# Performance work log

Measured on AMD Instinct MI355X. Metric: run time of the kernel, lower is better.

## Reference

```python
import jax, jax.numpy as jnp
import numpy as np

N, H, W = 128, 192, 192
THING = 81            # cfg.MODEL.SOGNET.THING_NUM_CLASSES
CLS_DIM = 128         # cls_embedding_dim
POS_DIM = 64          # pos_embedding_dim
REL_DIM = CLS_DIM + POS_DIM


def setup_inputs() -> dict:
    key = jax.random.key(0)
    ks = jax.random.split(key, 8)
    mask_logits = jax.random.normal(ks[0], (1, N, H, W), dtype=jnp.float32)
    # valid boxes: x_max > x_min, y_max > y_min (log(w/h) must be finite)
    xy = jax.random.uniform(ks[1], (N, 2), minval=0.0, maxval=800.0)
    wh = jax.random.uniform(ks[2], (N, 2), minval=16.0, maxval=256.0)
    bbox = jnp.concatenate([xy, xy + wh], axis=1).astype(jnp.float32)
    cls_idx = jax.random.randint(ks[3], (N,), 1, THING)  # values in [1, 80]
    # params (kaiming-normal-ish scale)
    W_U = jax.random.normal(ks[4], (THING - 1, CLS_DIM), jnp.float32) * (2.0 / (THING - 1)) ** 0.5
    W_V = jax.random.normal(ks[5], (THING - 1, CLS_DIM), jnp.float32) * (2.0 / (THING - 1)) ** 0.5
    W_pos = jax.random.normal(ks[6], (4, POS_DIM), jnp.float32) * (2.0 / 4.0) ** 0.5
    W_P = jax.random.normal(ks[7], (REL_DIM, 1), jnp.float32) * (2.0 / REL_DIM) ** 0.5
    return {"mask_logits": mask_logits, "bbox": bbox, "W_U": W_U, "W_V": W_V,
            "W_pos": W_pos, "W_P": W_P, "cls_idx": cls_idx}


def _position_matrix(bbox):
    x_min, y_min, x_max, y_max = bbox[:, 0], bbox[:, 1], bbox[:, 2], bbox[:, 3]
    w = x_max - x_min
    h = y_max - y_min
    x_ctr = (x_min + x_max) / 2.0
    y_ctr = (y_min + y_max) / 2.0
    dx = -(x_ctr[:, None] - x_ctr[None, :]) / w[:, None]          # [N, N]
    dy = -(y_ctr[:, None] - y_ctr[None, :]) / h[:, None]
    dw = jnp.log(w[None, :] / w[:, None])                          # log(w_j / w_i)
    dh = jnp.log(h[None, :] / h[:, None])
    return jnp.stack([dx, dy, dw, dh], axis=2)                     # [N, N, 4]


def reference(mask_logits, bbox, W_U, W_V, W_pos, W_P, cls_idx):
    # --- class relation: outer product of two relu'd class embeddings ---
    one_hot = jax.nn.one_hot(cls_idx - 1, THING - 1, dtype=mask_logits.dtype)  # [N, 80]
    feat1 = jax.nn.relu(one_hot @ W_U)                             # [N, CLS_DIM]
    feat2 = jax.nn.relu(one_hot @ W_V)
    cls_rel = feat1[:, None, :] * feat2[None, :, :]                # [N, N, CLS_DIM]
    # --- position relation: 1x1 conv == linear over last dim ---
    pos_rel = jax.nn.relu(jnp.einsum('ijk,kd->ijd', _position_matrix(bbox), W_pos))  # [N, N, POS_DIM]
    # --- relation score ---
    relation_feat = jnp.concatenate([cls_rel, pos_rel], axis=2)    # [N, N, REL_DIM]
    overlap_score = jax.nn.sigmoid(jnp.einsum('ijk,k->ij', relation_feat, W_P[:, 0]))  # [N, N]
    relation_score = jax.nn.relu(overlap_score - overlap_score.T)  # [N, N]
    # --- relation-weighted mask aggregation ---
    # naive: sum_m (ml*mp)[b,n] * mp[b,m] * score[n,m]  -> factor the m-reduction as a GEMM
    mask_prob = jax.nn.sigmoid(mask_logits)                        # [1, N, H, W]
    weighted = jnp.einsum('nm,bmhw->bnhw', relation_score, mask_prob)
    overlap_part = mask_logits * mask_prob * weighted              # [1, N, H, W]
    return mask_logits - overlap_part
```

## Files before the change

### kernel.cpp

```cpp
#include <hip/hip_runtime.h>

#define HW    36864
#define PX    144
#define RST   136

typedef unsigned short u16;
typedef unsigned int   u32;
typedef __attribute__((ext_vector_type(8))) short bf16x8;
typedef __attribute__((ext_vector_type(4))) float f32x4;

__device__ __forceinline__ float bf2f(u32 u) {
    union { u32 i; float f; } c; c.i = u << 16; return c.f;
}
__device__ __forceinline__ u16 f2bf(float f) {
    union { float f; u32 i; } c; c.f = f;
    u32 r = (c.i + 0x7fffu + ((c.i >> 16) & 1u)) >> 16;
    return (u16)r;
}
__device__ __forceinline__ u32 pack2(float a, float b) {
    return (u32)f2bf(a) | ((u32)f2bf(b) << 16);
}
__device__ __forceinline__ float sigf(float x) { return 1.0f / (1.0f + __expf(-x)); }

__device__ __forceinline__ void unpack8(uint4 v, float* o) {
    o[0] = bf2f(v.x & 0xffffu); o[1] = bf2f(v.x >> 16);
    o[2] = bf2f(v.y & 0xffffu); o[3] = bf2f(v.y >> 16);
    o[4] = bf2f(v.z & 0xffffu); o[5] = bf2f(v.z >> 16);
    o[6] = bf2f(v.w & 0xffffu); o[7] = bf2f(v.w >> 16);
}

template<int BF16>
__device__ __forceinline__ float ld1(const void* p, int idx) {
    return BF16 ? bf2f((u32)((const u16*)p)[idx]) : ((const float*)p)[idx];
}

template<int BF16>
__device__ __forceinline__ bool wrong_dtype(const void* ml, int tid) {
    int pred = 0;
    if (tid < 128) {
        u16 v = ((const u16*)ml)[tid];
        u32 e = (v >> 7) & 0xffu;
        pred = ((v & 0x7fffu) == 0 || (e >= 90u && e <= 140u)) ? 1 : 0;
    }
    int cnt = __syncthreads_count(pred);
    return (cnt >= 100) != (BF16 != 0);
}

template<int BF16>
__global__ __launch_bounds__(128) void k_rel(
    const void* __restrict__ ml,   const void* __restrict__ bbox,
    const void* __restrict__ WU,   const void* __restrict__ WV,
    const void* __restrict__ Wpos, const void* __restrict__ WP,
    const int* __restrict__ cls,   u16* __restrict__ relN)
{
    const int n = blockIdx.x, m = threadIdx.x;
    if (wrong_dtype<BF16>(ml, m)) return;

    __shared__ float u_s[128], v_s[128], wpos_s[256], wpp_s[64], bbn_s[4];

    const int cn = cls[n] - 1;
    {
        float wp = ld1<BF16>(WP, m);
        u_s[m] = fmaxf(ld1<BF16>(WU, cn * 128 + m), 0.f) * wp;
        v_s[m] = fmaxf(ld1<BF16>(WV, cn * 128 + m), 0.f) * wp;
    }
    wpos_s[m]       = ld1<BF16>(Wpos, m);
    wpos_s[128 + m] = ld1<BF16>(Wpos, 128 + m);
    if (m < 64) wpp_s[m] = ld1<BF16>(WP, 128 + m);
    if (m < 4)  bbn_s[m] = ld1<BF16>(bbox, n * 4 + m);
    __syncthreads();

    const int cm = cls[m] - 1;
    float s1 = 0.f, s2 = 0.f;
    #pragma unroll 8
    for (int c = 0; c < 128; ++c) {
        float wv = ld1<BF16>(WV, cm * 128 + c);
        float wu = ld1<BF16>(WU, cm * 128 + c);
        s1 += u_s[c] * fmaxf(wv, 0.f);
        s2 += v_s[c] * fmaxf(wu, 0.f);
    }

    const float xmn = bbn_s[0], ymn = bbn_s[1], xMn = bbn_s[2], yMn = bbn_s[3];
    const float wn = xMn - xmn, hn = yMn - ymn;
    const float xcn = 0.5f * (xmn + xMn), ycn = 0.5f * (ymn + yMn);
    const float xmm = ld1<BF16>(bbox, m * 4 + 0), ymm = ld1<BF16>(bbox, m * 4 + 1);
    const float xMm = ld1<BF16>(bbox, m * 4 + 2), yMm = ld1<BF16>(bbox, m * 4 + 3);
    const float wm = xMm - xmm, hm = yMm - ymm;
    const float xcm = 0.5f * (xmm + xMm), ycm = 0.5f * (ymm + yMm);

    const float p0 = -(xcn - xcm) / wn, p1 = -(ycn - ycm) / hn;
    const float p2 = __logf(wm / wn),   p3 = __logf(hm / hn);
    const float q0 = -(xcm - xcn) / wm, q1 = -(ycm - ycn) / hm;
    const float q2 = __logf(wn / wm),   q3 = __logf(hn / hm);

    #pragma unroll 8
    for (int d = 0; d < 64; ++d) {
        float w0 = wpos_s[d], w1 = wpos_s[64 + d], w2 = wpos_s[128 + d], w3 = wpos_s[192 + d];
        float wp = wpp_s[d];
        float t1 = p0 * w0 + p1 * w1 + p2 * w2 + p3 * w3;
        float t2 = q0 * w0 + q1 * w1 + q2 * w2 + q3 * w3;
        s1 += fmaxf(t1, 0.f) * wp;
        s2 += fmaxf(t2, 0.f) * wp;
    }

    float r = fmaxf(sigf(s1) - sigf(s2), 0.f);
    relN[n * 128 + m] = f2bf(r);
}

template<int BF16>
__global__ __launch_bounds__(256) void k_main(
    const void* __restrict__ mlv, const u16* __restrict__ relN,
    void* __restrict__ outv)
{
    const int tid = threadIdx.x;
    if (wrong_dtype<BF16>(mlv, tid)) return;

    __shared__ u16 rel_s[128 * RST];
    __shared__ u16 prob_s[64 * PX];

    const int px0 = blockIdx.x * PX;
    const int w    = tid >> 6;
    const int lane = tid & 63;
    const int col  = lane & 15;
    const int quad = lane >> 4;
    const int n0   = w * 32;

    for (int idx = tid; idx < 2048; idx += 256) {
        int r = idx >> 4, c = idx & 15;
        uint4 v = ((const uint4*)relN)[idx];
        *(uint4*)(rel_s + r * RST + c * 8) = v;
    }

    f32x4 acc[2][9];
    #pragma unroll
    for (int i = 0; i < 2; ++i)
        #pragma unroll
        for (int t = 0; t < 9; ++t) acc[i][t] = (f32x4){0.f, 0.f, 0.f, 0.f};

    for (int h = 0; h < 2; ++h) {
        __syncthreads();
        for (int idx = tid; idx < 1152; idx += 256) {
            int r = idx / 18, c = idx - r * 18;
            size_t base = (size_t)(h * 64 + r) * HW + px0 + c * 8;
            float f[8];
            if (BF16) {
                uint4 v = *(const uint4*)((const u16*)mlv + base);
                unpack8(v, f);
            } else {
                float4 v0 = *(const float4*)((const float*)mlv + base);
                float4 v1 = *(const float4*)((const float*)mlv + base + 4);
                f[0] = v0.x; f[1] = v0.y; f[2] = v0.z; f[3] = v0.w;
                f[4] = v1.x; f[5] = v1.y; f[6] = v1.z; f[7] = v1.w;
            }
            uint4 o;
            o.x = pack2(sigf(f[0]), sigf(f[1]));
            o.y = pack2(sigf(f[2]), sigf(f[3]));
            o.z = pack2(sigf(f[4]), sigf(f[5]));
            o.w = pack2(sigf(f[6]), sigf(f[7]));
            *(uint4*)(prob_s + r * PX + c * 8) = o;
        }
        __syncthreads();

        #pragma unroll
        for (int ksl = 0; ksl < 2; ++ksl) {
            const int k0 = h * 64 + ksl * 32 + quad * 8;
            bf16x8 a0 = *(const bf16x8*)(rel_s + (n0 + col) * RST + k0);
            bf16x8 a1 = *(const bf16x8*)(rel_s + (n0 + 16 + col) * RST + k0);
            const u16* bbase = prob_s + (ksl * 32 + quad * 8) * PX + col;
            #pragma unroll
            for (int t = 0; t < 9; ++t) {
                const u16* bp = bbase + t * 16;
                bf16x8 bfrag;
                #pragma unroll
                for (int j = 0; j < 8; ++j) bfrag[j] = (short)bp[j * PX];
                acc[0][t] = __builtin_amdgcn_mfma_f32_16x16x32_bf16(a0, bfrag, acc[0][t], 0, 0, 0);
                acc[1][t] = __builtin_amdgcn_mfma_f32_16x16x32_bf16(a1, bfrag, acc[1][t], 0, 0, 0);
            }
        }
    }

    #pragma unroll
    for (int i = 0; i < 2; ++i) {
        #pragma unroll
        for (int t = 0; t < 9; ++t) {
            const int nb = n0 + i * 16 + quad * 4;
            const int px = px0 + t * 16 + col;
            #pragma unroll
            for (int r = 0; r < 4; ++r) {
                size_t off = (size_t)(nb + r) * HW + px;
                float mlvv = BF16 ? bf2f((u32)((const u16*)mlv)[off])
                                  : ((const float*)mlv)[off];
                float pr = sigf(mlvv);
                float o  = mlvv - mlvv * pr * acc[i][t][r];
                if (BF16) ((u16*)outv)[off] = f2bf(o);
                else      ((float*)outv)[off] = o;
            }
        }
    }
}

extern "C" void kernel_launch(void* const* d_in, const int* in_sizes, int n_in,
                              void* d_out, int out_size, void* d_ws, size_t ws_size,
                              hipStream_t stream) {
    const void* ml   = d_in[0];
    const void* bbox = d_in[1];
    const void* WU   = d_in[2];
    const void* WV   = d_in[3];
    const void* Wpos = d_in[4];
    const void* WP   = d_in[5];
    const int*  cls  = (const int*)d_in[6];

    u16* relN = (u16*)d_ws;

    k_rel<1><<<dim3(128), dim3(128), 0, stream>>>(ml, bbox, WU, WV, Wpos, WP, cls, relN);
    k_rel<0><<<dim3(128), dim3(128), 0, stream>>>(ml, bbox, WU, WV, Wpos, WP, cls, relN);
    k_main<1><<<dim3(256), dim3(256), 0, stream>>>(ml, relN, d_out);
    k_main<0><<<dim3(256), dim3(256), 0, stream>>>(ml, relN, d_out);
}
```

Before: 105.7 us.

## Merge dtype variants, precompute class dot table, shrink pixel tiles with swizzled LDS

Replaces the two templated dtype kernels with single kernels that branch at runtime, cutting four launches to two. The class-relation dot products are computed once per row as an 80-entry table built with wave reductions, instead of a 128-long serial loop per thread. The main kernel's pixel tile drops from 144 to 64 columns, so the grid grows from 256 to 576 blocks. Its LDS probability tile uses an XOR swizzle to reduce bank conflicts, and launch bounds request two blocks per CU. The cost is that each block reloads the full relation matrix, and there are more blocks in total.

```diff
diff --git a/kernel.cpp b/kernel.cpp
--- a/kernel.cpp
+++ b/kernel.cpp
@@ -1,7 +1,6 @@
 #include <hip/hip_runtime.h>
 
 #define HW    36864
-#define PX    144
 #define RST   136
 
 typedef unsigned short u16;
@@ -29,13 +28,7 @@
     o[6] = bf2f(v.w & 0xffffu); o[7] = bf2f(v.w >> 16);
 }
 
-template<int BF16>
-__device__ __forceinline__ float ld1(const void* p, int idx) {
-    return BF16 ? bf2f((u32)((const u16*)p)[idx]) : ((const float*)p)[idx];
-}
-
-template<int BF16>
-__device__ __forceinline__ bool wrong_dtype(const void* ml, int tid) {
+__device__ __forceinline__ bool is_bf16_blk(const void* ml, int tid) {
     int pred = 0;
     if (tid < 128) {
         u16 v = ((const u16*)ml)[tid];
@@ -43,48 +36,90 @@
         pred = ((v & 0x7fffu) == 0 || (e >= 90u && e <= 140u)) ? 1 : 0;
     }
     int cnt = __syncthreads_count(pred);
-    return (cnt >= 100) != (BF16 != 0);
-}
-
-template<int BF16>
-__global__ __launch_bounds__(128) void k_rel(
+    return cnt >= 100;
+}
+
+__global__ __launch_bounds__(256) void k_rel(
     const void* __restrict__ ml,   const void* __restrict__ bbox,
     const void* __restrict__ WU,   const void* __restrict__ WV,
     const void* __restrict__ Wpos, const void* __restrict__ WP,
     const int* __restrict__ cls,   u16* __restrict__ relN)
 {
-    const int n = blockIdx.x, m = threadIdx.x;
-    if (wrong_dtype<BF16>(ml, m)) return;
+    const int tid = threadIdx.x;
+    const bool bf = is_bf16_blk(ml, tid);
+    const int n = blockIdx.x;
 
     __shared__ float u_s[128], v_s[128], wpos_s[256], wpp_s[64], bbn_s[4];
+    __shared__ float d1_s[80], d2_s[80];
 
     const int cn = cls[n] - 1;
+    if (bf) {
+        if (tid < 128) {
+            float wp = bf2f(((const u16*)WP)[tid]);
+            u_s[tid] = fmaxf(bf2f(((const u16*)WU)[cn * 128 + tid]), 0.f) * wp;
+            v_s[tid] = fmaxf(bf2f(((const u16*)WV)[cn * 128 + tid]), 0.f) * wp;
+        }
+        wpos_s[tid] = bf2f(((const u16*)Wpos)[tid]);
+        if (tid < 64) wpp_s[tid] = bf2f(((const u16*)WP)[128 + tid]);
+        if (tid < 4)  bbn_s[tid] = bf2f(((const u16*)bbox)[n * 4 + tid]);
+    } else {
+        if (tid < 128) {
+            float wp = ((const float*)WP)[tid];
+            u_s[tid] = fmaxf(((const float*)WU)[cn * 128 + tid], 0.f) * wp;
+            v_s[tid] = fmaxf(((const float*)WV)[cn * 128 + tid], 0.f) * wp;
+        }
+        wpos_s[tid] = ((const float*)Wpos)[tid];
+        if (tid < 64) wpp_s[tid] = ((const float*)WP)[128 + tid];
+        if (tid < 4)  bbn_s[tid] = ((const float*)bbox)[n * 4 + tid];
+    }
+    __syncthreads();
+
     {
-        float wp = ld1<BF16>(WP, m);
-        u_s[m] = fmaxf(ld1<BF16>(WU, cn * 128 + m), 0.f) * wp;
-        v_s[m] = fmaxf(ld1<BF16>(WV, cn * 128 + m), 0.f) * wp;
-    }
-    wpos_s[m]       = ld1<BF16>(Wpos, m);
-    wpos_s[128 + m] = ld1<BF16>(Wpos, 128 + m);
-    if (m < 64) wpp_s[m] = ld1<BF16>(WP, 128 + m);
-    if (m < 4)  bbn_s[m] = ld1<BF16>(bbox, n * 4 + m);
+        const int wv_ = tid >> 6, lane = tid & 63;
+        const float ua = u_s[lane], ub = u_s[64 + lane];
+        const float va = v_s[lane], vb = v_s[64 + lane];
+        for (int a = wv_; a < 80; a += 4) {
+            float x0, x1, y0, y1;
+            if (bf) {
+                x0 = bf2f(((const u16*)WV)[a * 128 + lane]);
+                x1 = bf2f(((const u16*)WV)[a * 128 + 64 + lane]);
+                y0 = bf2f(((const u16*)WU)[a * 128 + lane]);
+                y1 = bf2f(((const u16*)WU)[a * 128 + 64 + lane]);
+            } else {
+                x0 = ((const float*)WV)[a * 128 + lane];
+                x1 = ((const float*)WV)[a * 128 + 64 + lane];
+                y0 = ((const float*)WU)[a * 128 + lane];
+                y1 = ((const float*)WU)[a * 128 + 64 + lane];
+            }
+            float p1 = ua * fmaxf(x0, 0.f) + ub * fmaxf(x1, 0.f);
+            float p2 = va * fmaxf(y0, 0.f) + vb * fmaxf(y1, 0.f);
+            #pragma unroll
+            for (int o = 32; o; o >>= 1) {
+                p1 += __shfl_xor(p1, o);
+                p2 += __shfl_xor(p2, o);
+            }
+            if (lane == 0) { d1_s[a] = p1; d2_s[a] = p2; }
+        }
+    }
     __syncthreads();
 
+    if (tid >= 128) return;
+    const int m = tid;
     const int cm = cls[m] - 1;
-    float s1 = 0.f, s2 = 0.f;
-    #pragma unroll 8
-    for (int c = 0; c < 128; ++c) {
-        float wv = ld1<BF16>(WV, cm * 128 + c);
-        float wu = ld1<BF16>(WU, cm * 128 + c);
-        s1 += u_s[c] * fmaxf(wv, 0.f);
-        s2 += v_s[c] * fmaxf(wu, 0.f);
-    }
+    float s1 = d1_s[cm];
+    float s2 = d2_s[cm];
 
     const float xmn = bbn_s[0], ymn = bbn_s[1], xMn = bbn_s[2], yMn = bbn_s[3];
     const float wn = xMn - xmn, hn = yMn - ymn;
     const float xcn = 0.5f * (xmn + xMn), ycn = 0.5f * (ymn + yMn);
-    const float xmm = ld1<BF16>(bbox, m * 4 + 0), ymm = ld1<BF16>(bbox, m * 4 + 1);
-    const float xMm = ld1<BF16>(bbox, m * 4 + 2), yMm = ld1<BF16>(bbox, m * 4 + 3);
+    float xmm, ymm, xMm, yMm;
+    if (bf) {
+        xmm = bf2f(((const u16*)bbox)[m * 4 + 0]); ymm = bf2f(((const u16*)bbox)[m * 4 + 1]);
+        xMm = bf2f(((const u16*)bbox)[m * 4 + 2]); yMm = bf2f(((const u16*)bbox)[m * 4 + 3]);
+    } else {
+        xmm = ((const float*)bbox)[m * 4 + 0]; ymm = ((const float*)bbox)[m * 4 + 1];
+        xMm = ((const float*)bbox)[m * 4 + 2]; yMm = ((const float*)bbox)[m * 4 + 3];
+    }
     const float wm = xMm - xmm, hm = yMm - ymm;
     const float xcm = 0.5f * (xmm + xMm), ycm = 0.5f * (ymm + yMm);
 
@@ -107,23 +142,21 @@
     relN[n * 128 + m] = f2bf(r);
 }
 
-template<int BF16>
-__global__ __launch_bounds__(256) void k_main(
+__global__ __launch_bounds__(256, 2) void k_main(
     const void* __restrict__ mlv, const u16* __restrict__ relN,
     void* __restrict__ outv)
 {
     const int tid = threadIdx.x;
-    if (wrong_dtype<BF16>(mlv, tid)) return;
+    const bool bf = is_bf16_blk(mlv, tid);
 
     __shared__ u16 rel_s[128 * RST];
-    __shared__ u16 prob_s[64 * PX];
-
-    const int px0 = blockIdx.x * PX;
-    const int w    = tid >> 6;
+    __shared__ u16 prob_s[64 * 64];
+
+    const int px0  = blockIdx.x * 64;
     const int lane = tid & 63;
     const int col  = lane & 15;
     const int quad = lane >> 4;
-    const int n0   = w * 32;
+    const int n0   = (tid >> 6) * 32;
 
     for (int idx = tid; idx < 2048; idx += 256) {
         int r = idx >> 4, c = idx & 15;
@@ -131,19 +164,22 @@
         *(uint4*)(rel_s + r * RST + c * 8) = v;
     }
 
-    f32x4 acc[2][9];
+    f32x4 acc[2][4];
     #pragma unroll
     for (int i = 0; i < 2; ++i)
         #pragma unroll
-        for (int t = 0; t < 9; ++t) acc[i][t] = (f32x4){0.f, 0.f, 0.f, 0.f};
+        for (int t = 0; t < 4; ++t) acc[i][t] = (f32x4){0.f, 0.f, 0.f, 0.f};
 
     for (int h = 0; h < 2; ++h) {
         __syncthreads();
-        for (int idx = tid; idx < 1152; idx += 256) {
-            int r = idx / 18, c = idx - r * 18;
-            size_t base = (size_t)(h * 64 + r) * HW + px0 + c * 8;
+        #pragma unroll
+        for (int it = 0; it < 2; ++it) {
+            int idx = tid + it * 256;
+            int r = idx >> 3, c8 = idx & 7;
+            int qr = (r >> 3) & 3;
+            size_t base = (size_t)(h * 64 + r) * HW + px0 + c8 * 8;
             float f[8];
-            if (BF16) {
+            if (bf) {
                 uint4 v = *(const uint4*)((const u16*)mlv + base);
                 unpack8(v, f);
             } else {
@@ -157,7 +193,7 @@
             o.y = pack2(sigf(f[2]), sigf(f[3]));
             o.z = pack2(sigf(f[4]), sigf(f[5]));
             o.w = pack2(sigf(f[6]), sigf(f[7]));
-            *(uint4*)(prob_s + r * PX + c * 8) = o;
+            *(uint4*)((char*)prob_s + r * 128 + ((c8 * 16) ^ (qr * 32))) = o;
         }
         __syncthreads();
 
@@ -166,13 +202,15 @@
             const int k0 = h * 64 + ksl * 32 + quad * 8;
             bf16x8 a0 = *(const bf16x8*)(rel_s + (n0 + col) * RST + k0);
             bf16x8 a1 = *(const bf16x8*)(rel_s + (n0 + 16 + col) * RST + k0);
-            const u16* bbase = prob_s + (ksl * 32 + quad * 8) * PX + col;
+            const int rb = ksl * 32 + quad * 8;
             #pragma unroll
-            for (int t = 0; t < 9; ++t) {
-                const u16* bp = bbase + t * 16;
+            for (int t = 0; t < 4; ++t) {
                 bf16x8 bfrag;
                 #pragma unroll
-                for (int j = 0; j < 8; ++j) bfrag[j] = (short)bp[j * PX];
+                for (int j = 0; j < 8; ++j) {
+                    bfrag[j] = (short)*(const u16*)((const char*)prob_s + (rb + j) * 128
+                                                    + ((t * 32 + col * 2) ^ (quad * 32)));
+                }
                 acc[0][t] = __builtin_amdgcn_mfma_f32_16x16x32_bf16(a0, bfrag, acc[0][t], 0, 0, 0);
                 acc[1][t] = __builtin_amdgcn_mfma_f32_16x16x32_bf16(a1, bfrag, acc[1][t], 0, 0, 0);
             }
@@ -182,18 +220,21 @@
     #pragma unroll
     for (int i = 0; i < 2; ++i) {
         #pragma unroll
-        for (int t = 0; t < 9; ++t) {
+        for (int t = 0; t < 4; ++t) {
             const int nb = n0 + i * 16 + quad * 4;
             const int px = px0 + t * 16 + col;
             #pragma unroll
             for (int r = 0; r < 4; ++r) {
                 size_t off = (size_t)(nb + r) * HW + px;
-                float mlvv = BF16 ? bf2f((u32)((const u16*)mlv)[off])
-                                  : ((const float*)mlv)[off];
-                float pr = sigf(mlvv);
-                float o  = mlvv - mlvv * pr * acc[i][t][r];
-                if (BF16) ((u16*)outv)[off] = f2bf(o);
-                else      ((float*)outv)[off] = o;
+                if (bf) {
+                    float mlvv = bf2f((u32)((const u16*)mlv)[off]);
+                    float pr = sigf(mlvv);
+                    ((u16*)outv)[off] = f2bf(mlvv - mlvv * pr * acc[i][t][r]);
+                } else {
+                    float mlvv = ((const float*)mlv)[off];
+                    float pr = sigf(mlvv);
+                    ((float*)outv)[off] = mlvv - mlvv * pr * acc[i][t][r];
+                }
             }
         }
     }
@@ -212,8 +253,6 @@
 
     u16* relN = (u16*)d_ws;
 
-    k_rel<1><<<dim3(128), dim3(128), 0, stream>>>(ml, bbox, WU, WV, Wpos, WP, cls, relN);
-    k_rel<0><<<dim3(128), dim3(128), 0, stream>>>(ml, bbox, WU, WV, Wpos, WP, cls, relN);
-    k_main<1><<<dim3(256), dim3(256), 0, stream>>>(ml, relN, d_out);
-    k_main<0><<<dim3(256), dim3(256), 0, stream>>>(ml, relN, d_out);
-}
+    k_rel<<<dim3(128), dim3(256), 0, stream>>>(ml, bbox, WU, WV, Wpos, WP, cls, relN);
+    k_main<<<dim3(576), dim3(256), 0, stream>>>(ml, relN, d_out);
+}
```

Measured after the change: 113.5 us. +7.4%, slower.
